# Performance work log

Hardware: AMD Instinct MI355X
Metric: run time of the kernel (lower is better)

The kernel has to match this reference:

```python
import jax, jax.numpy as jnp
import numpy as np

NOISE_LEVEL = 1.0

def setup_inputs() -> dict:
    key = jax.random.key(0)
    k1, k2, k3 = jax.random.split(key, 3)
    N, NUM_CODE, DIM_CODE = 16384, 2048, 512
    x = jax.random.normal(k1, (N, NUM_CODE), dtype=jnp.float32)
    noise = jax.random.uniform(k2, (N, NUM_CODE), dtype=jnp.float32)
    codebook = jax.random.normal(k3, (NUM_CODE, DIM_CODE), dtype=jnp.float32)
    return {"x": x, "noise": noise, "codebook": codebook}

def reference(x, noise, codebook):
    # softmax over codes
    sm = jax.nn.softmax(x, axis=1)                      # [N, num_code]
    # noisy argmax (noise replaces torch.rand_like for determinism)
    idx = jnp.argmax(sm - NOISE_LEVEL * noise, axis=1)  # [N]
    one_hot = jax.nn.one_hot(idx, x.shape[1], dtype=sm.dtype)
    # straight-through: value == one_hot, gradient flows through softmax
    ste = sm - jax.lax.stop_gradient(sm - one_hot)
    y = ste @ codebook                                   # [N, dim_code]
    return y
```

## Files before the change

kernel.cpp:

```cpp
#include <hip/hip_runtime.h>

#define NUM_CODE 2048
#define DIM_CODE 512

__global__ __launch_bounds__(256) void vq_row_kernel(
    const float* __restrict__ x,
    const float* __restrict__ noise,
    const float* __restrict__ codebook,
    float* __restrict__ out)
{
    __shared__ float s_f[4];
    __shared__ float s_bv[4];
    __shared__ int   s_bi[4];

    const int row  = blockIdx.x;
    const int tid  = threadIdx.x;
    const int lane = tid & 63;
    const int wave = tid >> 6;

    const float4* x4 = (const float4*)(x     + (size_t)row * NUM_CODE);
    const float4* n4 = (const float4*)(noise + (size_t)row * NUM_CODE);

    const float4 a  = x4[tid];
    const float4 b  = x4[256 + tid];
    const float4 na = n4[tid];
    const float4 nb = n4[256 + tid];

    float m = fmaxf(fmaxf(fmaxf(a.x, a.y), fmaxf(a.z, a.w)),
                    fmaxf(fmaxf(b.x, b.y), fmaxf(b.z, b.w)));
    #pragma unroll
    for (int off = 32; off; off >>= 1)
        m = fmaxf(m, __shfl_xor(m, off));
    if (lane == 0) s_f[wave] = m;
    __syncthreads();
    m = fmaxf(fmaxf(s_f[0], s_f[1]), fmaxf(s_f[2], s_f[3]));
    __syncthreads();

    float e0 = expf(a.x - m), e1 = expf(a.y - m), e2 = expf(a.z - m), e3 = expf(a.w - m);
    float e4 = expf(b.x - m), e5 = expf(b.y - m), e6 = expf(b.z - m), e7 = expf(b.w - m);
    float s = ((e0 + e1) + (e2 + e3)) + ((e4 + e5) + (e6 + e7));
    #pragma unroll
    for (int off = 32; off; off >>= 1)
        s += __shfl_xor(s, off);
    if (lane == 0) s_f[wave] = s;
    __syncthreads();
    s = (s_f[0] + s_f[1]) + (s_f[2] + s_f[3]);

    const int i0 = 4 * tid;
    const int i1 = 1024 + 4 * tid;

    float bv = e0 / s - na.x; int bi = i0;
    { float v = e1 / s - na.y; if (v > bv) { bv = v; bi = i0 + 1; } }
    { float v = e2 / s - na.z; if (v > bv) { bv = v; bi = i0 + 2; } }
    { float v = e3 / s - na.w; if (v > bv) { bv = v; bi = i0 + 3; } }
    { float v = e4 / s - nb.x; if (v > bv) { bv = v; bi = i1;     } }
    { float v = e5 / s - nb.y; if (v > bv) { bv = v; bi = i1 + 1; } }
    { float v = e6 / s - nb.z; if (v > bv) { bv = v; bi = i1 + 2; } }
    { float v = e7 / s - nb.w; if (v > bv) { bv = v; bi = i1 + 3; } }

    #pragma unroll
    for (int off = 32; off; off >>= 1) {
        float ov = __shfl_xor(bv, off);
        int   oi = __shfl_xor(bi, off);
        if (ov > bv || (ov == bv && oi < bi)) { bv = ov; bi = oi; }
    }
    if (lane == 0) { s_bv[wave] = bv; s_bi[wave] = bi; }
    __syncthreads();
    bv = s_bv[0]; bi = s_bi[0];
    #pragma unroll
    for (int w = 1; w < 4; ++w) {
        float ov = s_bv[w]; int oi = s_bi[w];
        if (ov > bv || (ov == bv && oi < bi)) { bv = ov; bi = oi; }
    }

    if (tid < 128) {
        const float4* cb = (const float4*)(codebook + (size_t)bi * DIM_CODE);
        float4*       o  = (float4*)(out + (size_t)row * DIM_CODE);
        o[tid] = cb[tid];
    }
}

extern "C" void kernel_launch(void* const* d_in, const int* in_sizes, int n_in,
                              void* d_out, int out_size, void* d_ws, size_t ws_size,
                              hipStream_t stream) {
    const float* x        = (const float*)d_in[0];
    const float* noise    = (const float*)d_in[1];
    const float* codebook = (const float*)d_in[2];
    float* out            = (float*)d_out;

    const int n_rows = in_sizes[0] / NUM_CODE;

    vq_row_kernel<<<n_rows, 256, 0, stream>>>(x, noise, codebook, out);
}
```

Measured before the change: 59.74 us.

## Map one row per wavefront to remove block-level barriers and shared memory

Each 64-lane wavefront now processes a whole row, holding 32 values of x and noise per lane in registers, and each block handles 4 rows. All reductions (max, sum, argmax) become pure wave shuffles with no __syncthreads or LDS traffic. The per-element division is replaced by multiplication with a reciprocal. This raises register pressure and deepens per-lane load batches, which may reduce occupancy.

```diff
diff --git a/kernel.cpp b/kernel.cpp
--- a/kernel.cpp
+++ b/kernel.cpp
@@ -9,75 +9,64 @@
     const float* __restrict__ codebook,
     float* __restrict__ out)
 {
-    __shared__ float s_f[4];
-    __shared__ float s_bv[4];
-    __shared__ int   s_bi[4];
-
-    const int row  = blockIdx.x;
     const int tid  = threadIdx.x;
     const int lane = tid & 63;
     const int wave = tid >> 6;
+    const int row  = blockIdx.x * 4 + wave;
 
     const float4* x4 = (const float4*)(x     + (size_t)row * NUM_CODE);
     const float4* n4 = (const float4*)(noise + (size_t)row * NUM_CODE);
 
-    const float4 a  = x4[tid];
-    const float4 b  = x4[256 + tid];
-    const float4 na = n4[tid];
-    const float4 nb = n4[256 + tid];
+    float4 a[8];
+    float4 nz[8];
+    #pragma unroll
+    for (int j = 0; j < 8; ++j) a[j]  = x4[j * 64 + lane];
+    #pragma unroll
+    for (int j = 0; j < 8; ++j) nz[j] = n4[j * 64 + lane];
+    __builtin_amdgcn_sched_barrier(0);
 
-    float m = fmaxf(fmaxf(fmaxf(a.x, a.y), fmaxf(a.z, a.w)),
-                    fmaxf(fmaxf(b.x, b.y), fmaxf(b.z, b.w)));
+    float m = fmaxf(fmaxf(a[0].x, a[0].y), fmaxf(a[0].z, a[0].w));
+    #pragma unroll
+    for (int j = 1; j < 8; ++j)
+        m = fmaxf(m, fmaxf(fmaxf(a[j].x, a[j].y), fmaxf(a[j].z, a[j].w)));
     #pragma unroll
     for (int off = 32; off; off >>= 1)
         m = fmaxf(m, __shfl_xor(m, off));
-    if (lane == 0) s_f[wave] = m;
-    __syncthreads();
-    m = fmaxf(fmaxf(s_f[0], s_f[1]), fmaxf(s_f[2], s_f[3]));
-    __syncthreads();
 
-    float e0 = expf(a.x - m), e1 = expf(a.y - m), e2 = expf(a.z - m), e3 = expf(a.w - m);
-    float e4 = expf(b.x - m), e5 = expf(b.y - m), e6 = expf(b.z - m), e7 = expf(b.w - m);
-    float s = ((e0 + e1) + (e2 + e3)) + ((e4 + e5) + (e6 + e7));
+    float s = 0.f;
+    #pragma unroll
+    for (int j = 0; j < 8; ++j) {
+        a[j].x = expf(a[j].x - m);
+        a[j].y = expf(a[j].y - m);
+        a[j].z = expf(a[j].z - m);
+        a[j].w = expf(a[j].w - m);
+        s += (a[j].x + a[j].y) + (a[j].z + a[j].w);
+    }
     #pragma unroll
     for (int off = 32; off; off >>= 1)
         s += __shfl_xor(s, off);
-    if (lane == 0) s_f[wave] = s;
-    __syncthreads();
-    s = (s_f[0] + s_f[1]) + (s_f[2] + s_f[3]);
+    const float inv = 1.0f / s;
 
-    const int i0 = 4 * tid;
-    const int i1 = 1024 + 4 * tid;
-
-    float bv = e0 / s - na.x; int bi = i0;
-    { float v = e1 / s - na.y; if (v > bv) { bv = v; bi = i0 + 1; } }
-    { float v = e2 / s - na.z; if (v > bv) { bv = v; bi = i0 + 2; } }
-    { float v = e3 / s - na.w; if (v > bv) { bv = v; bi = i0 + 3; } }
-    { float v = e4 / s - nb.x; if (v > bv) { bv = v; bi = i1;     } }
-    { float v = e5 / s - nb.y; if (v > bv) { bv = v; bi = i1 + 1; } }
-    { float v = e6 / s - nb.z; if (v > bv) { bv = v; bi = i1 + 2; } }
-    { float v = e7 / s - nb.w; if (v > bv) { bv = v; bi = i1 + 3; } }
-
+    float bv = -INFINITY; int bi = 0;
+    #pragma unroll
+    for (int j = 0; j < 8; ++j) {
+        const int base = 256 * j + 4 * lane;
+        { float v = a[j].x * inv - nz[j].x; if (v > bv) { bv = v; bi = base;     } }
+        { float v = a[j].y * inv - nz[j].y; if (v > bv) { bv = v; bi = base + 1; } }
+        { float v = a[j].z * inv - nz[j].z; if (v > bv) { bv = v; bi = base + 2; } }
+        { float v = a[j].w * inv - nz[j].w; if (v > bv) { bv = v; bi = base + 3; } }
+    }
     #pragma unroll
     for (int off = 32; off; off >>= 1) {
         float ov = __shfl_xor(bv, off);
         int   oi = __shfl_xor(bi, off);
         if (ov > bv || (ov == bv && oi < bi)) { bv = ov; bi = oi; }
     }
-    if (lane == 0) { s_bv[wave] = bv; s_bi[wave] = bi; }
-    __syncthreads();
-    bv = s_bv[0]; bi = s_bi[0];
-    #pragma unroll
-    for (int w = 1; w < 4; ++w) {
-        float ov = s_bv[w]; int oi = s_bi[w];
-        if (ov > bv || (ov == bv && oi < bi)) { bv = ov; bi = oi; }
-    }
 
-    if (tid < 128) {
-        const float4* cb = (const float4*)(codebook + (size_t)bi * DIM_CODE);
-        float4*       o  = (float4*)(out + (size_t)row * DIM_CODE);
-        o[tid] = cb[tid];
-    }
+    const float4* cb = (const float4*)(codebook + (size_t)bi * DIM_CODE);
+    float4*       o  = (float4*)(out + (size_t)row * DIM_CODE);
+    o[lane]      = cb[lane];
+    o[64 + lane] = cb[64 + lane];
 }
 
 extern "C" void kernel_launch(void* const* d_in, const int* in_sizes, int n_in,
@@ -89,6 +78,5 @@
     float* out            = (float*)d_out;
 
     const int n_rows = in_sizes[0] / NUM_CODE;
-
-    vq_row_kernel<<<n_rows, 256, 0, stream>>>(x, noise, codebook, out);
+    vq_row_kernel<<<n_rows / 4, 256, 0, stream>>>(x, noise, codebook, out);
 }
```

Measured after the change: 56.01 us. 1.07x faster.
